# Kernel tuning notes

Measured on AMD Instinct MI355X. Metric: run time of the kernel, lower is better.

The kernel has to match this reference:

```python
import jax, jax.numpy as jnp
import numpy as np

N_HEAD = 20
ALIGN_HEAD_IDX = (4, 7, 11)  # heads of alignment_heads with layer_idx == layer_index (2)


def setup_inputs() -> dict:
    key = jax.random.key(0)
    ks = jax.random.split(key, 7)
    B, Tq, Tk, D = 8, 448, 1500, 1280
    s = 1.0 / np.sqrt(D)
    return {
        "x": jax.random.normal(ks[0], (B, Tq, D), jnp.float32),
        "k": jax.random.normal(ks[1], (B, Tk, D), jnp.float32),
        "v": jax.random.normal(ks[2], (B, Tk, D), jnp.float32),
        "Wq": jax.random.normal(ks[3], (D, D), jnp.float32) * s,
        "bq": jax.random.normal(ks[4], (D,), jnp.float32) * 0.02,
        "Wo": jax.random.normal(ks[5], (D, D), jnp.float32) * s,
        "bo": jax.random.normal(ks[6], (D,), jnp.float32) * 0.02,
    }


def reference(x, k, v, Wq, bq, Wo, bo):
    B, Tq, D = x.shape
    H = N_HEAD
    Dh = D // H
    scale = Dh ** (-0.25)

    # q projection (torch Linear: x @ W.T + b)
    q = x @ Wq.T + bq                                   # [B, Tq, D]
    qh = q.reshape(B, Tq, H, Dh).transpose(0, 2, 1, 3)  # [B, H, Tq, Dh]
    kh = k.reshape(B, -1, H, Dh).transpose(0, 2, 1, 3)  # [B, H, Tk, Dh]
    vh = v.reshape(B, -1, H, Dh).transpose(0, 2, 1, 3)  # [B, H, Tk, Dh]

    # scaled QK^T, softmax in fp32
    qk = jnp.einsum("bhqd,bhkd->bhqk", qh * scale, kh * scale)
    w = jax.nn.softmax(qk.astype(jnp.float32), axis=-1).astype(q.dtype)

    out = jnp.einsum("bhqk,bhkd->bhqd", w, vh)          # [B, H, Tq, Dh]
    out = out.transpose(0, 2, 1, 3).reshape(B, Tq, D)
    out = out @ Wo.T + bo

    alignment_weights = w[:, jnp.array(ALIGN_HEAD_IDX), :, :]  # [B, 3, Tq, Tk]
    return out, alignment_weights
```

## Files before the change

### kernel.cpp

```cpp
#include <hip/hip_runtime.h>
#include <stdint.h>


typedef short bf16x8 __attribute__((ext_vector_type(8)));
typedef float f32x4  __attribute__((ext_vector_type(4)));

#define VMCNT(n) asm volatile("s_waitcnt vmcnt(" #n ")" ::: "memory")

__device__ __forceinline__ unsigned short f2bf(float f) {
  union { float f; unsigned int u; } c; c.f = f;
  unsigned int u = c.u;
  unsigned int r = (u + 0x7FFFu + ((u >> 16) & 1u)) >> 16;
  return (unsigned short)r;
}

__device__ __forceinline__ float exp2_hw(float x) {
  float r;
  asm("v_exp_f32 %0, %1" : "=v"(r) : "v"(x));
  return r;
}

__device__ __forceinline__ void gld_lds16(const void* g, void* l) {
  __builtin_amdgcn_global_load_lds(
      (__attribute__((address_space(1))) void*)g,
      (__attribute__((address_space(3))) void*)l, 16, 0, 0);
}

__device__ __forceinline__ int swz128(int row, int c16) {
  return (row << 7) + ((c16 ^ (row & 7)) << 4);
}

__device__ __forceinline__ bf16x8 ldfrag(const unsigned short* base, int row, int c16) {
  return *reinterpret_cast<const bf16x8*>(
      reinterpret_cast<const char*>(base) + swz128(row, c16));
}

__global__ __launch_bounds__(256) void cvt_kernel(const float* __restrict__ src,
                                                  unsigned short* __restrict__ dst,
                                                  long n) {
  long i = ((long)blockIdx.x * 256 + threadIdx.x) * 4;
  if (i + 3 < n) {
    float4 v = *reinterpret_cast<const float4*>(src + i);
    ushort4 o;
    o.x = f2bf(v.x); o.y = f2bf(v.y); o.z = f2bf(v.z); o.w = f2bf(v.w);
    *reinterpret_cast<ushort4*>(dst + i) = o;
  }
}

__global__ __launch_bounds__(256) void vt_kernel(const float* __restrict__ v,
                                                 unsigned short* __restrict__ vbt) {
  __shared__ float T[64][65];
  int blk = blockIdx.x;
  const int kt = blk % 24; blk /= 24;
  const int h = blk % 20; const int b = blk / 20;
  const int tid = threadIdx.x;
  const int c  = tid & 63;
  const int r0 = tid >> 6;
#pragma unroll
  for (int r = 0; r < 16; ++r) {
    const int tk = r * 4 + r0;
    const int gtk = kt * 64 + tk;
    float val = 0.f;
    if (gtk < 1500) val = v[(size_t)(b * 1500 + gtk) * 1280 + h * 64 + c];
    T[tk][c] = val;
  }
  __syncthreads();
#pragma unroll
  for (int r = 0; r < 16; ++r) {
    const int d = r * 4 + r0;
    vbt[((size_t)(b * 20 + h) * 64 + d) * 1536 + kt * 64 + c] = f2bf(T[c][d]);
  }
}

template <int EPI>
__global__ __launch_bounds__(256) void gemm_bt(const unsigned short* __restrict__ A,
                                               const unsigned short* __restrict__ Bm,
                                               const float* __restrict__ bias,
                                               void* __restrict__ Cout,
                                               int M, int N, int K, float scale) {
  __shared__ __attribute__((aligned(16))) unsigned short As[128 * 64];
  __shared__ __attribute__((aligned(16))) unsigned short Bs[128 * 64];
  const int tid = threadIdx.x;
  const int w = tid >> 6, lane = tid & 63;
  const int l15 = lane & 15, l4 = lane >> 4;
  const int nBlk = N >> 7;
  const int cpx = gridDim.x >> 3;
  const int bid = (blockIdx.x & 7) * cpx + (blockIdx.x >> 3);
  const int bm = bid / nBlk, bn = bid % nBlk;
  const int m0 = bm << 7, n0 = bn << 7;
  const int wr = (w >> 1) << 6, wc = (w & 1) << 6;

  f32x4 acc[4][4] = {};

  const int nKt = K >> 6;
  for (int kt = 0; kt < nKt; ++kt) {
    const int koff = kt << 6;
#pragma unroll
    for (int r = 0; r < 4; ++r) {
      const int base = (((w << 2) + r) << 10);
      const int p = base + (lane << 4);
      const int row = p >> 7;
      const int cb = (p & 127) >> 1;
      gld_lds16(A  + ((size_t)(m0 + row) * K + koff + cb), (char*)As + base);
      gld_lds16(Bm + ((size_t)(n0 + row) * K + koff + cb), (char*)Bs + base);
    }
    __syncthreads();
#pragma unroll
    for (int kk = 0; kk < 64; kk += 32) {
      bf16x8 af[4], bfr[4];
#pragma unroll
      for (int mi = 0; mi < 4; ++mi)
        af[mi] = *reinterpret_cast<const bf16x8*>(&As[(wr + mi * 16 + l15) * 64 + kk + l4 * 8]);
#pragma unroll
      for (int ni = 0; ni < 4; ++ni)
        bfr[ni] = *reinterpret_cast<const bf16x8*>(&Bs[(wc + ni * 16 + l15) * 64 + kk + l4 * 8]);
#pragma unroll
      for (int mi = 0; mi < 4; ++mi)
#pragma unroll
        for (int ni = 0; ni < 4; ++ni)
          acc[mi][ni] = __builtin_amdgcn_mfma_f32_16x16x32_bf16(af[mi], bfr[ni], acc[mi][ni], 0, 0, 0);
    }
    __syncthreads();
  }
#pragma unroll
  for (int ni = 0; ni < 4; ++ni) {
    const int n = n0 + wc + ni * 16 + l15;
    const float bv = bias[n];
#pragma unroll
    for (int mi = 0; mi < 4; ++mi) {
#pragma unroll
      for (int i = 0; i < 4; ++i) {
        const int m = m0 + wr + mi * 16 + l4 * 4 + i;
        float vv = (acc[mi][ni][i] + bv) * scale;
        if (EPI == 0)
          ((unsigned short*)Cout)[(size_t)m * N + n] = f2bf(vv);
        else
          ((float*)Cout)[(size_t)m * N + n] = vv;
      }
    }
  }
}

__global__ __launch_bounds__(256) void attn_kernel(const unsigned short* __restrict__ Qg,
                                                   const unsigned short* __restrict__ Kg,
                                                   const unsigned short* __restrict__ Vtg,
                                                   unsigned short* __restrict__ Og,
                                                   float* __restrict__ ML) {
  __shared__ __attribute__((aligned(16))) unsigned short Qs[64 * 64];
  __shared__ __attribute__((aligned(16))) unsigned short Ps[64 * 64];
  __shared__ __attribute__((aligned(16))) unsigned short Ks0[64 * 64];
  __shared__ __attribute__((aligned(16))) unsigned short Vs0[64 * 64];
  __shared__ __attribute__((aligned(16))) unsigned short Ks1[64 * 64];
  __shared__ __attribute__((aligned(16))) unsigned short Vs1[64 * 64];
  const int tid = threadIdx.x;
  const int w = tid >> 6, lane = tid & 63;
  const int l15 = lane & 15, l4 = lane >> 4;
  int bid = (blockIdx.x & 7) * 140 + (blockIdx.x >> 3);
  const int qt = bid % 7; bid /= 7;
  const int h = bid % 20; const int b = bid / 20;
  const int tq0 = qt << 6;

  const int srow = lane >> 3;
  const int scol = ((lane & 7) ^ srow) << 3;
  const size_t vbase = ((size_t)(b * 20 + h)) * 64 * 1536;
  const int pfbase = w * 2048 + ((l4 >> 1) << 8) + (l15 << 4) + ((l4 & 1) << 3);

#pragma unroll
  for (int c = 0; c < 2; ++c) {
    const int ch = w * 2 + c;
    const int row = ch * 8 + srow;
    gld_lds16(Qg + ((size_t)(b * 448 + tq0 + row) * 1280 + h * 64 + scol),
              (char*)Qs + ch * 1024);
  }
#pragma unroll
  for (int c = 0; c < 2; ++c) {
    const int ch = w * 2 + c;
    const int row = ch * 8 + srow;
    int tk = row; if (tk > 1499) tk = 1499;
    gld_lds16(Kg + ((size_t)(b * 1500 + tk) * 1280 + h * 64 + scol), (char*)Ks0 + ch * 1024);
    gld_lds16(Vtg + (vbase + (size_t)row * 1536 + scol), (char*)Vs0 + ch * 1024);
  }
  VMCNT(0);
  __builtin_amdgcn_s_barrier();

  float l_part = 0.f;
  f32x4 o_acc[4] = {};

  for (int kt = 0; kt < 24; ++kt) {
    const int cur = kt & 1;
    const unsigned short* Kb = cur ? Ks1 : Ks0;
    const unsigned short* Vb = cur ? Vs1 : Vs0;
    unsigned short* Kn = cur ? Ks0 : Ks1;
    unsigned short* Vn = cur ? Vs0 : Vs1;

    if (kt < 23) {
      const int k0n = (kt + 1) << 6;
#pragma unroll
      for (int c = 0; c < 2; ++c) {
        const int ch = w * 2 + c;
        const int row = ch * 8 + srow;
        int tk = k0n + row; if (tk > 1499) tk = 1499;
        gld_lds16(Kg + ((size_t)(b * 1500 + tk) * 1280 + h * 64 + scol), (char*)Kn + ch * 1024);
        gld_lds16(Vtg + (vbase + (size_t)row * 1536 + k0n + scol), (char*)Vn + ch * 1024);
      }
      VMCNT(4);
    } else {
      VMCNT(0);
    }
    __builtin_amdgcn_s_barrier();

    f32x4 s[4] = {};
    __builtin_amdgcn_s_setprio(1);
#pragma unroll
    for (int h2 = 0; h2 < 2; ++h2) {
      bf16x8 qf = ldfrag(Qs, w * 16 + l15, h2 * 4 + l4);
#pragma unroll
      for (int ni = 0; ni < 4; ++ni) {
        bf16x8 kf = ldfrag(Kb, ni * 16 + l15, h2 * 4 + l4);
        s[ni] = __builtin_amdgcn_mfma_f32_16x16x32_bf16(kf, qf, s[ni], 0, 0, 0);
      }
    }
    __builtin_amdgcn_s_setprio(0);

    if (kt == 23) {
#pragma unroll
      for (int ni = 0; ni < 4; ++ni) {
        const int kb = ni * 16 + l4 * 4;
#pragma unroll
        for (int i = 0; i < 4; ++i)
          if (kb + i >= 28) s[ni][i] = -1e30f;
      }
    }

#pragma unroll
    for (int ni = 0; ni < 4; ++ni) {
#pragma unroll
      for (int i = 0; i < 4; ++i) {
        float e = exp2_hw(fmaf(s[ni][i], 1.44269504f, -17.31234049f));
        s[ni][i] = e;
        l_part += e;
      }
    }

#pragma unroll
    for (int ni = 0; ni < 4; ++ni) {
#pragma unroll
      for (int ip = 0; ip < 2; ++ip) {
        unsigned int u;
        asm("v_cvt_pk_bf16_f32 %0, %1, %2"
            : "=v"(u) : "v"(s[ni][2 * ip]), "v"(s[ni][2 * ip + 1]));
        *reinterpret_cast<unsigned int*>(
            (char*)Ps + pfbase + ((ni >> 1) << 10) + ((ni & 1) << 9) + (ip << 2)) = u;
      }
    }

    __builtin_amdgcn_s_setprio(1);
#pragma unroll
    for (int h2 = 0; h2 < 2; ++h2) {
      bf16x8 ap = *reinterpret_cast<const bf16x8*>(
          (char*)Ps + w * 2048 + (h2 << 10) + (lane << 4));
#pragma unroll
      for (int nd = 0; nd < 4; ++nd) {
        bf16x8 bv = ldfrag(Vb, nd * 16 + l15, h2 * 4 + l4);
        o_acc[nd] = __builtin_amdgcn_mfma_f32_16x16x32_bf16(ap, bv, o_acc[nd], 0, 0, 0);
      }
    }
    __builtin_amdgcn_s_setprio(0);
    __builtin_amdgcn_s_barrier();
  }

  float lt = l_part + __shfl_xor(l_part, 16);
  lt += __shfl_xor(lt, 32);
  float lrow[4], rinv[4];
#pragma unroll
  for (int i = 0; i < 4; ++i) {
    lrow[i] = __shfl(lt, l4 * 4 + i);
    rinv[i] = 1.f / lrow[i];
  }
#pragma unroll
  for (int nd = 0; nd < 4; ++nd)
#pragma unroll
    for (int i = 0; i < 4; ++i) {
      int row = w * 16 + l4 * 4 + i;
      Og[(size_t)(b * 448 + tq0 + row) * 1280 + h * 64 + nd * 16 + l15] =
          f2bf(o_acc[nd][i] * rinv[i]);
    }
  if (l15 == 0) {
#pragma unroll
    for (int i = 0; i < 4; ++i) {
      int row = w * 16 + l4 * 4 + i;
      size_t idx = (size_t)(b * 20 + h) * 448 + tq0 + row;
      ML[idx * 2]     = 12.0f;
      ML[idx * 2 + 1] = lrow[i];
    }
  }
}

__global__ __launch_bounds__(256) void weights_kernel(const unsigned short* __restrict__ Qg,
                                                      const unsigned short* __restrict__ Kg,
                                                      const float* __restrict__ ML,
                                                      float* __restrict__ Wout) {
  __shared__ __attribute__((aligned(16))) unsigned short Qs[64 * 64];
  __shared__ __attribute__((aligned(16))) unsigned short Ks0[64 * 64];
  __shared__ __attribute__((aligned(16))) unsigned short Ks1[64 * 64];
  const int tid = threadIdx.x;
  const int w = tid >> 6, lane = tid & 63;
  const int l15 = lane & 15, l4 = lane >> 4;
  int bid = (blockIdx.x & 7) * 21 + (blockIdx.x >> 3);
  const int qt = bid % 7; bid /= 7;
  const int ha = bid % 3; const int b = bid / 3;
  const int h = (ha == 0) ? 4 : (ha == 1) ? 7 : 11;
  const int tq0 = qt << 6;

  const int srow = lane >> 3;
  const int scol = ((lane & 7) ^ srow) << 3;

#pragma unroll
  for (int c = 0; c < 2; ++c) {
    const int ch = w * 2 + c;
    const int row = ch * 8 + srow;
    gld_lds16(Qg + ((size_t)(b * 448 + tq0 + row) * 1280 + h * 64 + scol),
              (char*)Qs + ch * 1024);
  }
#pragma unroll
  for (int c = 0; c < 2; ++c) {
    const int ch = w * 2 + c;
    const int row = ch * 8 + srow;
    int tk = row; if (tk > 1499) tk = 1499;
    gld_lds16(Kg + ((size_t)(b * 1500 + tk) * 1280 + h * 64 + scol), (char*)Ks0 + ch * 1024);
  }
  VMCNT(0);
  __builtin_amdgcn_s_barrier();

  float m_r[4], rinv[4];
#pragma unroll
  for (int i = 0; i < 4; ++i) {
    size_t idx = (size_t)(b * 20 + h) * 448 + tq0 + w * 16 + l4 * 4 + i;
    m_r[i]  = ML[idx * 2];
    rinv[i] = 1.f / ML[idx * 2 + 1];
  }
  float* wbase = Wout + ((size_t)(b * 3 + ha) * 448 + tq0) * 1500;

  for (int kt = 0; kt < 24; ++kt) {
    const int cur = kt & 1;
    const unsigned short* Kb = cur ? Ks1 : Ks0;
    unsigned short* Kn = cur ? Ks0 : Ks1;
    if (kt < 23) {
      const int k0n = (kt + 1) << 6;
#pragma unroll
      for (int c = 0; c < 2; ++c) {
        const int ch = w * 2 + c;
        const int row = ch * 8 + srow;
        int tk = k0n + row; if (tk > 1499) tk = 1499;
        gld_lds16(Kg + ((size_t)(b * 1500 + tk) * 1280 + h * 64 + scol), (char*)Kn + ch * 1024);
      }
      VMCNT(2);
    } else {
      VMCNT(0);
    }
    __builtin_amdgcn_s_barrier();

    f32x4 s[4] = {};
    __builtin_amdgcn_s_setprio(1);
#pragma unroll
    for (int h2 = 0; h2 < 2; ++h2) {
      bf16x8 aq = ldfrag(Qs, w * 16 + l15, h2 * 4 + l4);
#pragma unroll
      for (int ni = 0; ni < 4; ++ni) {
        bf16x8 bk = ldfrag(Kb, ni * 16 + l15, h2 * 4 + l4);
        s[ni] = __builtin_amdgcn_mfma_f32_16x16x32_bf16(aq, bk, s[ni], 0, 0, 0);
      }
    }
    __builtin_amdgcn_s_setprio(0);

    const int k0 = kt << 6;
#pragma unroll
    for (int ni = 0; ni < 4; ++ni) {
      const int col = k0 + ni * 16 + l15;
      if (col < 1500) {
#pragma unroll
        for (int i = 0; i < 4; ++i) {
          const int row = w * 16 + l4 * 4 + i;
          wbase[(size_t)row * 1500 + col] = __expf(s[ni][i] - m_r[i]) * rinv[i];
        }
      }
    }
    __builtin_amdgcn_s_barrier();
  }
}

extern "C" void kernel_launch(void* const* d_in, const int* in_sizes, int n_in,
                              void* d_out, int out_size, void* d_ws, size_t ws_size,
                              hipStream_t stream) {
  const float* x  = (const float*)d_in[0];
  const float* k  = (const float*)d_in[1];
  const float* v  = (const float*)d_in[2];
  const float* Wq = (const float*)d_in[3];
  const float* bq = (const float*)d_in[4];
  const float* Wo = (const float*)d_in[5];
  const float* bo = (const float*)d_in[6];
  float* out  = (float*)d_out;
  float* wout = out + (size_t)8 * 448 * 1280;

  char* ws = (char*)d_ws;
  unsigned short* xb  = (unsigned short*)(ws);
  unsigned short* wqb = (unsigned short*)(ws + 9175040);
  unsigned short* wob = (unsigned short*)(ws + 12451840);
  unsigned short* kb  = (unsigned short*)(ws + 15728640);
  unsigned short* vbt = (unsigned short*)(ws + 46448640);
  unsigned short* qs  = (unsigned short*)(ws + 77905920);
  unsigned short* ao  = (unsigned short*)(ws + 87080960);
  float* ml           = (float*)(ws + 96256000);

  cvt_kernel<<<4480, 256, 0, stream>>>(x,  xb,  (long)4587520);
  cvt_kernel<<<1600, 256, 0, stream>>>(Wq, wqb, (long)1638400);
  cvt_kernel<<<1600, 256, 0, stream>>>(Wo, wob, (long)1638400);
  cvt_kernel<<<15000, 256, 0, stream>>>(k, kb,  (long)15360000);
  vt_kernel<<<3840, 256, 0, stream>>>(v, vbt);

  gemm_bt<0><<<280, 256, 0, stream>>>(xb, wqb, bq, (void*)qs, 3584, 1280, 1280, 0.125f);

  attn_kernel<<<8 * 20 * 7, 256, 0, stream>>>(qs, kb, vbt, ao, ml);

  gemm_bt<1><<<280, 256, 0, stream>>>(ao, wob, bo, (void*)out, 3584, 1280, 1280, 1.0f);

  weights_kernel<<<8 * 3 * 7, 256, 0, stream>>>(qs, kb, ml, wout);
}
```

Measured before the change: 204.6 us.

## Merge conversion launches, keep Q fragments in registers, widen P stores

Replaces the four separate fp32-to-bf16 conversion launches with a single kernel that selects its source and destination by block index, removing launch overhead and tail gaps. In the attention and weights kernels, Q fragments are now loaded straight from global memory into registers instead of being staged through LDS. This frees shared memory and removes repeated LDS fragment reads inside the loop. The P tile is written with 64-bit stores instead of two 32-bit stores, and the attention kernel gets a launch-bounds occupancy hint, which could limit registers and cause spills.

```diff
diff --git a/kernel.cpp b/kernel.cpp
--- a/kernel.cpp
+++ b/kernel.cpp
@@ -35,16 +35,21 @@
       reinterpret_cast<const char*>(base) + swz128(row, c16));
 }
 
-__global__ __launch_bounds__(256) void cvt_kernel(const float* __restrict__ src,
-                                                  unsigned short* __restrict__ dst,
-                                                  long n) {
-  long i = ((long)blockIdx.x * 256 + threadIdx.x) * 4;
-  if (i + 3 < n) {
-    float4 v = *reinterpret_cast<const float4*>(src + i);
-    ushort4 o;
-    o.x = f2bf(v.x); o.y = f2bf(v.y); o.z = f2bf(v.z); o.w = f2bf(v.w);
-    *reinterpret_cast<ushort4*>(dst + i) = o;
-  }
+__global__ __launch_bounds__(256) void cvt4_kernel(const float* __restrict__ s0, unsigned short* __restrict__ d0,
+                                                   const float* __restrict__ s1, unsigned short* __restrict__ d1,
+                                                   const float* __restrict__ s2, unsigned short* __restrict__ d2,
+                                                   const float* __restrict__ s3, unsigned short* __restrict__ d3) {
+  int blk = blockIdx.x;
+  const float* src; unsigned short* dst;
+  if (blk < 4480)       { src = s0; dst = d0; }
+  else if (blk < 6080)  { src = s1; dst = d1; blk -= 4480; }
+  else if (blk < 7680)  { src = s2; dst = d2; blk -= 6080; }
+  else                  { src = s3; dst = d3; blk -= 7680; }
+  long i = ((long)blk * 256 + threadIdx.x) * 4;
+  float4 v = *reinterpret_cast<const float4*>(src + i);
+  ushort4 o;
+  o.x = f2bf(v.x); o.y = f2bf(v.y); o.z = f2bf(v.z); o.w = f2bf(v.w);
+  *reinterpret_cast<ushort4*>(dst + i) = o;
 }
 
 __global__ __launch_bounds__(256) void vt_kernel(const float* __restrict__ v,
@@ -141,12 +146,11 @@
   }
 }
 
-__global__ __launch_bounds__(256) void attn_kernel(const unsigned short* __restrict__ Qg,
-                                                   const unsigned short* __restrict__ Kg,
-                                                   const unsigned short* __restrict__ Vtg,
-                                                   unsigned short* __restrict__ Og,
-                                                   float* __restrict__ ML) {
-  __shared__ __attribute__((aligned(16))) unsigned short Qs[64 * 64];
+__global__ __launch_bounds__(256, 4) void attn_kernel(const unsigned short* __restrict__ Qg,
+                                                      const unsigned short* __restrict__ Kg,
+                                                      const unsigned short* __restrict__ Vtg,
+                                                      unsigned short* __restrict__ Og,
+                                                      float* __restrict__ ML) {
   __shared__ __attribute__((aligned(16))) unsigned short Ps[64 * 64];
   __shared__ __attribute__((aligned(16))) unsigned short Ks0[64 * 64];
   __shared__ __attribute__((aligned(16))) unsigned short Vs0[64 * 64];
@@ -165,13 +169,12 @@
   const size_t vbase = ((size_t)(b * 20 + h)) * 64 * 1536;
   const int pfbase = w * 2048 + ((l4 >> 1) << 8) + (l15 << 4) + ((l4 & 1) << 3);
 
-#pragma unroll
-  for (int c = 0; c < 2; ++c) {
-    const int ch = w * 2 + c;
-    const int row = ch * 8 + srow;
-    gld_lds16(Qg + ((size_t)(b * 448 + tq0 + row) * 1280 + h * 64 + scol),
-              (char*)Qs + ch * 1024);
-  }
+  const unsigned short* qptr =
+      Qg + (size_t)(b * 448 + tq0 + w * 16 + l15) * 1280 + h * 64 + l4 * 8;
+  bf16x8 qreg[2];
+  qreg[0] = *reinterpret_cast<const bf16x8*>(qptr);
+  qreg[1] = *reinterpret_cast<const bf16x8*>(qptr + 32);
+
 #pragma unroll
   for (int c = 0; c < 2; ++c) {
     const int ch = w * 2 + c;
@@ -213,11 +216,10 @@
     __builtin_amdgcn_s_setprio(1);
 #pragma unroll
     for (int h2 = 0; h2 < 2; ++h2) {
-      bf16x8 qf = ldfrag(Qs, w * 16 + l15, h2 * 4 + l4);
 #pragma unroll
       for (int ni = 0; ni < 4; ++ni) {
         bf16x8 kf = ldfrag(Kb, ni * 16 + l15, h2 * 4 + l4);
-        s[ni] = __builtin_amdgcn_mfma_f32_16x16x32_bf16(kf, qf, s[ni], 0, 0, 0);
+        s[ni] = __builtin_amdgcn_mfma_f32_16x16x32_bf16(kf, qreg[h2], s[ni], 0, 0, 0);
       }
     }
     __builtin_amdgcn_s_setprio(0);
@@ -244,14 +246,12 @@
 
 #pragma unroll
     for (int ni = 0; ni < 4; ++ni) {
-#pragma unroll
-      for (int ip = 0; ip < 2; ++ip) {
-        unsigned int u;
-        asm("v_cvt_pk_bf16_f32 %0, %1, %2"
-            : "=v"(u) : "v"(s[ni][2 * ip]), "v"(s[ni][2 * ip + 1]));
-        *reinterpret_cast<unsigned int*>(
-            (char*)Ps + pfbase + ((ni >> 1) << 10) + ((ni & 1) << 9) + (ip << 2)) = u;
-      }
+      unsigned int u0, u1;
+      asm("v_cvt_pk_bf16_f32 %0, %1, %2" : "=v"(u0) : "v"(s[ni][0]), "v"(s[ni][1]));
+      asm("v_cvt_pk_bf16_f32 %0, %1, %2" : "=v"(u1) : "v"(s[ni][2]), "v"(s[ni][3]));
+      unsigned long long u01 = ((unsigned long long)u1 << 32) | u0;
+      *reinterpret_cast<unsigned long long*>(
+          (char*)Ps + pfbase + ((ni >> 1) << 10) + ((ni & 1) << 9)) = u01;
     }
 
     __builtin_amdgcn_s_setprio(1);
@@ -300,7 +300,6 @@
                                                       const unsigned short* __restrict__ Kg,
                                                       const float* __restrict__ ML,
                                                       float* __restrict__ Wout) {
-  __shared__ __attribute__((aligned(16))) unsigned short Qs[64 * 64];
   __shared__ __attribute__((aligned(16))) unsigned short Ks0[64 * 64];
   __shared__ __attribute__((aligned(16))) unsigned short Ks1[64 * 64];
   const int tid = threadIdx.x;
@@ -315,13 +314,12 @@
   const int srow = lane >> 3;
   const int scol = ((lane & 7) ^ srow) << 3;
 
-#pragma unroll
-  for (int c = 0; c < 2; ++c) {
-    const int ch = w * 2 + c;
-    const int row = ch * 8 + srow;
-    gld_lds16(Qg + ((size_t)(b * 448 + tq0 + row) * 1280 + h * 64 + scol),
-              (char*)Qs + ch * 1024);
-  }
+  const unsigned short* qptr =
+      Qg + (size_t)(b * 448 + tq0 + w * 16 + l15) * 1280 + h * 64 + l4 * 8;
+  bf16x8 qreg[2];
+  qreg[0] = *reinterpret_cast<const bf16x8*>(qptr);
+  qreg[1] = *reinterpret_cast<const bf16x8*>(qptr + 32);
+
 #pragma unroll
   for (int c = 0; c < 2; ++c) {
     const int ch = w * 2 + c;
@@ -364,11 +362,10 @@
     __builtin_amdgcn_s_setprio(1);
 #pragma unroll
     for (int h2 = 0; h2 < 2; ++h2) {
-      bf16x8 aq = ldfrag(Qs, w * 16 + l15, h2 * 4 + l4);
 #pragma unroll
       for (int ni = 0; ni < 4; ++ni) {
         bf16x8 bk = ldfrag(Kb, ni * 16 + l15, h2 * 4 + l4);
-        s[ni] = __builtin_amdgcn_mfma_f32_16x16x32_bf16(aq, bk, s[ni], 0, 0, 0);
+        s[ni] = __builtin_amdgcn_mfma_f32_16x16x32_bf16(qreg[h2], bk, s[ni], 0, 0, 0);
       }
     }
     __builtin_amdgcn_s_setprio(0);
@@ -412,10 +409,7 @@
   unsigned short* ao  = (unsigned short*)(ws + 87080960);
   float* ml           = (float*)(ws + 96256000);
 
-  cvt_kernel<<<4480, 256, 0, stream>>>(x,  xb,  (long)4587520);
-  cvt_kernel<<<1600, 256, 0, stream>>>(Wq, wqb, (long)1638400);
-  cvt_kernel<<<1600, 256, 0, stream>>>(Wo, wob, (long)1638400);
-  cvt_kernel<<<15000, 256, 0, stream>>>(k, kb,  (long)15360000);
+  cvt4_kernel<<<22680, 256, 0, stream>>>(x, xb, Wq, wqb, Wo, wob, k, kb);
   vt_kernel<<<3840, 256, 0, stream>>>(v, vbt);
 
   gemm_bt<0><<<280, 256, 0, stream>>>(xb, wqb, bq, (void*)qs, 3584, 1280, 1280, 0.125f);
```

After: 188.4 us. -7.9%, faster.
